# Kernel tuning notes

Hardware: AMD Instinct MI355X
Metric: run time of the kernel (lower is better)

## Reference

```python
import jax, jax.numpy as jnp
import numpy as np

B, N, D, M, C = 4, 256, 128, 128, 128


def _lin_init(key, din, dout):
    # torch nn.Linear default: U(-1/sqrt(din), 1/sqrt(din)) for weight and bias
    bound = 1.0 / np.sqrt(din)
    kw, kb = jax.random.split(key)
    W = jax.random.uniform(kw, (din, dout), jnp.float32, -bound, bound)
    b = jax.random.uniform(kb, (dout,), jnp.float32, -bound, bound)
    return W, b


def setup_inputs() -> dict:
    key = jax.random.key(0)
    k_h, k_adj, k1, k2, k3, k4 = jax.random.split(key, 6)
    h = jax.random.normal(k_h, (B, N, D), jnp.float32)
    adj = jax.random.uniform(k_adj, (B, N, N), jnp.float32)
    # msg MLP: Linear(2D -> M), SiLU, Linear(M -> M). Split first weight into
    # the h_i block (W1a) and h_j block (W1b) of the concatenated input.
    W1, b1 = _lin_init(k1, 2 * D, M)
    W1a, W1b = W1[:D], W1[D:]
    W2, b2 = _lin_init(k2, M, M)
    # to_c MLP: Linear(M -> M), SiLU, Linear(M -> C)
    Wc1, bc1 = _lin_init(k3, M, M)
    Wc2, bc2 = _lin_init(k4, M, C)
    return {"h": h, "adj": adj, "W1a": W1a, "W1b": W1b, "b1": b1,
            "W2": W2, "b2": b2, "Wc1": Wc1, "bc1": bc1, "Wc2": Wc2, "bc2": bc2}


def reference(h, adj, W1a, W1b, b1, W2, b2, Wc1, bc1, Wc2, bc2):
    n = h.shape[1]
    # First msg Linear on cat([h_i, h_j]) == h_i @ W1a + h_j @ W1b + b1.
    # Precompute per-node projections once instead of the (B,N,N,2D) pair tensor.
    pi = jnp.einsum('bnd,dm->bnm', h, W1a)           # (B,N,M) for destination i
    pj = jnp.einsum('bnd,dm->bnm', h, W1b)           # (B,N,M) for source j
    pre = pi[:, :, None, :] + pj[:, None, :, :] + b1  # (B,N,N,M)
    m = jnp.einsum('bijm,mk->bijk', jax.nn.silu(pre), W2) + b2  # (B,N,N,M)
    # zero self-messages (diagonal ignored), then weight by adjacency
    mask = (1.0 - jnp.eye(n, dtype=h.dtype))[None, :, :, None]
    m = m * mask * adj[..., None]
    # mean aggregation over source nodes j with clamped degree
    denom = jnp.clip(jnp.sum(adj, axis=-1, keepdims=True), 1.0)  # (B,N,1)
    m_agg = jnp.sum(m, axis=2) / denom                           # (B,N,M)
    c = jnp.einsum('bnm,mc->bnc', jax.nn.silu(jnp.einsum('bnm,mk->bnk', m_agg, Wc1) + bc1), Wc2) + bc2
    return c
```

## Files before the change

kernel.cpp:

```cpp
#include <hip/hip_runtime.h>
#include <math.h>

#define BB 4
#define NN 256
#define DD 128
#define MM 128
#define CC 128
#define ROWS (BB * NN)
#define RPB 4
#define NBLK (ROWS / RPB)
#define TPB 512

static __device__ __forceinline__ float fast_exp2(float x) {
#if __has_builtin(__builtin_amdgcn_exp2f)
    return __builtin_amdgcn_exp2f(x);
#else
    return __exp2f(x);
#endif
}

static __device__ __forceinline__ float fast_rcp(float x) {
#if __has_builtin(__builtin_amdgcn_rcpf)
    return __builtin_amdgcn_rcpf(x);
#else
    return 1.0f / x;
#endif
}

static __device__ __forceinline__ float silu_f(float x) {
    float e = fast_exp2(-1.44269504088896340736f * x);
    return x * fast_rcp(1.0f + e);
}

__global__ __launch_bounds__(TPB) void k_proj(const float* __restrict__ h,
                                              const float* __restrict__ W1a,
                                              const float* __restrict__ W1b,
                                              const float* __restrict__ b1,
                                              float* __restrict__ pibias,
                                              float* __restrict__ pj) {
    __shared__ float sWa[64 * MM];
    __shared__ float sWb[64 * MM];
    __shared__ float sH[RPB * DD];

    const int t = threadIdx.x;
    const int m = t & 127;
    const int q = t >> 7;
    const int row0 = blockIdx.x * RPB;

    const float bias = b1[m];

    sH[t] = h[(size_t)row0 * DD + t];

    float accA = 0.0f, accB = 0.0f;
    for (int c = 0; c < 2; ++c) {
        __syncthreads();
        const float4* ga = (const float4*)(W1a + (size_t)c * 64 * MM);
        const float4* gb = (const float4*)(W1b + (size_t)c * 64 * MM);
        float4* la = (float4*)sWa;
        float4* lb = (float4*)sWb;
        #pragma unroll
        for (int i = 0; i < 4; ++i) {
            la[t + TPB * i] = ga[t + TPB * i];
            lb[t + TPB * i] = gb[t + TPB * i];
        }
        __syncthreads();

        #pragma unroll 8
        for (int dd = 0; dd < 64; ++dd) {
            const float hv = sH[q * DD + c * 64 + dd];
            accA = fmaf(hv, sWa[dd * MM + m], accA);
            accB = fmaf(hv, sWb[dd * MM + m], accB);
        }
    }

    pibias[(size_t)row0 * MM + t] = accA + bias;
    pj[(size_t)row0 * MM + t]     = accB;
}

__global__ __launch_bounds__(TPB) void k_msgout(const float* __restrict__ adj,
                                                const float* __restrict__ pibias,
                                                const float* __restrict__ pj,
                                                const float* __restrict__ W2,
                                                const float* __restrict__ b2,
                                                const float* __restrict__ Wc1,
                                                const float* __restrict__ bc1,
                                                const float* __restrict__ Wc2,
                                                const float* __restrict__ bc2,
                                                float* __restrict__ out) {
    __shared__ float sStage[64 * MM];
    __shared__ float sAdj[RPB][NN];
    __shared__ float sS[RPB * MM];
    __shared__ float sB[RPB * MM];
    __shared__ float sWred0[8];
    __shared__ float sWred1[8];

    const int t = threadIdx.x;
    const int blk = blockIdx.x;
    const int b = blk >> 6;
    const int i0 = (blk & 63) * RPB;
    const int row0 = b * NN + i0;

    const int m = t & 127;
    const int q = t >> 7;
    const int w = t >> 6;

    const float b2k  = b2[m];
    const float bc1k = bc1[m];
    const float bc2k = bc2[m];
    const float pim  = pibias[(size_t)(row0 + q) * MM + m];

    const float* arow = adj + (size_t)row0 * NN;
    const float a0v = arow[t];
    const float a1v = arow[t + TPB];
    float* sA = &sAdj[0][0];
    sA[t] = a0v;
    sA[t + TPB] = a1v;

    float v0 = a0v, v1 = a1v;
    #pragma unroll
    for (int off = 32; off > 0; off >>= 1) {
        v0 += __shfl_xor(v0, off, 64);
        v1 += __shfl_xor(v1, off, 64);
    }
    if ((t & 63) == 0) { sWred0[w] = v0; sWred1[w] = v1; }
    __syncthreads();

    float A;
    if (q < 2) {
        const int base = (q & 1) * 4;
        A = sWred0[base] + sWred0[base + 1] + sWred0[base + 2] + sWred0[base + 3];
    } else {
        const int base = (q & 1) * 4;
        A = sWred1[base] + sWred1[base + 1] + sWred1[base + 2] + sWred1[base + 3];
    }
    const float aii = sAdj[q][i0 + q];
    __syncthreads();
    if (t < RPB) sAdj[t][i0 + t] = 0.0f;

    const float inv  = 1.0f / fmaxf(A, 1.0f);
    const float bet  = (A - aii) * inv;
    const float npim = -1.44269504088896340736f * pim;

    const float* __restrict__ pjB = pj + (size_t)b * NN * MM;
    float acc = 0.0f;
    for (int c = 0; c < 4; ++c) {
        __syncthreads();
        const float4* g = (const float4*)(pjB + (size_t)c * 64 * MM);
        float4* l = (float4*)sStage;
        #pragma unroll
        for (int i = 0; i < 4; ++i) l[t + TPB * i] = g[t + TPB * i];
        __syncthreads();

        #pragma unroll 8
        for (int jj = 0; jj < 64; ++jj) {
            const float pjv = sStage[jj * MM + m];
            const float wgt = sAdj[q][c * 64 + jj];
            const float x   = pim + pjv;
            const float e   = fast_exp2(fmaf(-1.44269504088896340736f, pjv, npim));
            acc = fmaf(wgt, x * fast_rcp(1.0f + e), acc);
        }
    }
    sS[q * MM + m] = acc * inv;


    float acc2 = bet * b2k;
    for (int c = 0; c < 2; ++c) {
        __syncthreads();
        const float4* g = (const float4*)(W2 + (size_t)c * 64 * MM);
        float4* l = (float4*)sStage;
        #pragma unroll
        for (int i = 0; i < 4; ++i) l[t + TPB * i] = g[t + TPB * i];
        __syncthreads();
        #pragma unroll 8
        for (int dd = 0; dd < 64; ++dd) {
            acc2 = fmaf(sS[q * MM + c * 64 + dd], sStage[dd * MM + m], acc2);
        }
    }
    sB[q * MM + m] = acc2;

    acc2 = bc1k;
    for (int c = 0; c < 2; ++c) {
        __syncthreads();
        const float4* g = (const float4*)(Wc1 + (size_t)c * 64 * MM);
        float4* l = (float4*)sStage;
        #pragma unroll
        for (int i = 0; i < 4; ++i) l[t + TPB * i] = g[t + TPB * i];
        __syncthreads();
        #pragma unroll 8
        for (int dd = 0; dd < 64; ++dd) {
            acc2 = fmaf(sB[q * MM + c * 64 + dd], sStage[dd * MM + m], acc2);
        }
    }
    sS[q * MM + m] = silu_f(acc2);

    acc2 = bc2k;
    for (int c = 0; c < 2; ++c) {
        __syncthreads();
        const float4* g = (const float4*)(Wc2 + (size_t)c * 64 * MM);
        float4* l = (float4*)sStage;
        #pragma unroll
        for (int i = 0; i < 4; ++i) l[t + TPB * i] = g[t + TPB * i];
        __syncthreads();
        #pragma unroll 8
        for (int dd = 0; dd < 64; ++dd) {
            acc2 = fmaf(sS[q * MM + c * 64 + dd], sStage[dd * MM + m], acc2);
        }
    }
    out[(size_t)row0 * CC + t] = acc2;
}

extern "C" void kernel_launch(void* const* d_in, const int* in_sizes, int n_in,
                              void* d_out, int out_size, void* d_ws, size_t ws_size,
                              hipStream_t stream) {
    const float* h   = (const float*)d_in[0];
    const float* adj = (const float*)d_in[1];
    const float* W1a = (const float*)d_in[2];
    const float* W1b = (const float*)d_in[3];
    const float* b1  = (const float*)d_in[4];
    const float* W2  = (const float*)d_in[5];
    const float* b2  = (const float*)d_in[6];
    const float* Wc1 = (const float*)d_in[7];
    const float* bc1 = (const float*)d_in[8];
    const float* Wc2 = (const float*)d_in[9];
    const float* bc2 = (const float*)d_in[10];
    float* out = (float*)d_out;

    float* ws = (float*)d_ws;
    float* pibias = ws;
    float* pj     = ws + (size_t)ROWS * MM;

    k_proj<<<NBLK, TPB, 0, stream>>>(h, W1a, W1b, b1, pibias, pj);
    k_msgout<<<NBLK, TPB, 0, stream>>>(adj, pibias, pj, W2, b2, Wc1, bc1,
                                       Wc2, bc2, out);
}
```

Before: 99.29 us.

## Stage full pj and weights via async global-to-LDS loads, overlapping with compute

Both kernels now stage their whole operand into a large LDS buffer using global_load_lds direct-to-LDS loads, instead of looping over 64-row chunks with a sync pair per chunk. In k_msgout, the next weight matrix (W2, Wc1, Wc2) is prefetched into the half of the buffer no longer being read, so the load overlaps the remaining message or GEMV work. Other changes: self-messages are removed by subtracting the diagonal term instead of zeroing adjacency, and two SiLU reciprocals share a single rcp. The cost is about 130KB of LDS per block, which limits occupancy to one block per CU. Correctness also depends on the async LDS loads having completed before each barrier.

```diff
diff --git a/kernel.cpp b/kernel.cpp
--- a/kernel.cpp
+++ b/kernel.cpp
@@ -11,6 +11,8 @@
 #define NBLK (ROWS / RPB)
 #define TPB 512
 
+#define L2E 1.44269504088896340736f
+
 static __device__ __forceinline__ float fast_exp2(float x) {
 #if __has_builtin(__builtin_amdgcn_exp2f)
     return __builtin_amdgcn_exp2f(x);
@@ -28,8 +30,35 @@
 }
 
 static __device__ __forceinline__ float silu_f(float x) {
-    float e = fast_exp2(-1.44269504088896340736f * x);
+    float e = fast_exp2(-L2E * x);
     return x * fast_rcp(1.0f + e);
+}
+
+#if __has_builtin(__builtin_amdgcn_global_load_lds)
+#define HAS_GLDS 1
+#define GLDS(gp, lp)                                                        \
+    __builtin_amdgcn_global_load_lds(                                       \
+        (const __attribute__((address_space(1))) void*)(gp),                \
+        (__attribute__((address_space(3))) void*)(lp), 16, 0, 0)
+#else
+#define HAS_GLDS 0
+#endif
+
+template <int ITERS>
+static __device__ __forceinline__ void stage_lin(float* lds, const float* g,
+                                                 int t) {
+#if HAS_GLDS
+    const int wv = t >> 6, lane = t & 63;
+    #pragma unroll
+    for (int i = 0; i < ITERS; ++i) {
+        const int c = i * 8 + wv;
+        GLDS(g + (size_t)c * 256 + lane * 4, lds + c * 256);
+    }
+#else
+    #pragma unroll
+    for (int i = 0; i < ITERS; ++i)
+        ((float4*)lds)[i * TPB + t] = ((const float4*)g)[i * TPB + t];
+#endif
 }
 
 __global__ __launch_bounds__(TPB) void k_proj(const float* __restrict__ h,
@@ -38,8 +67,7 @@
                                               const float* __restrict__ b1,
                                               float* __restrict__ pibias,
                                               float* __restrict__ pj) {
-    __shared__ float sWa[64 * MM];
-    __shared__ float sWb[64 * MM];
+    __shared__ float sW[128 * 256];
     __shared__ float sH[RPB * DD];
 
     const int t = threadIdx.x;
@@ -47,30 +75,45 @@
     const int q = t >> 7;
     const int row0 = blockIdx.x * RPB;
 
+    sH[t] = h[(size_t)row0 * DD + t];
+
+#if HAS_GLDS
+    {
+        const int wv = t >> 6, lane = t & 63;
+        #pragma unroll
+        for (int i = 0; i < 16; ++i) {
+            const int r = i * 8 + wv;
+            const float* g = (lane < 32)
+                                 ? (W1a + (size_t)r * 128 + lane * 4)
+                                 : (W1b + (size_t)r * 128 + (lane - 32) * 4);
+            GLDS(g, &sW[r * 256]);
+        }
+    }
+#else
+    #pragma unroll
+    for (int i = 0; i < 16; ++i) {
+        const int f = i * TPB + t;
+        const int r = f >> 6;
+        const int c4 = f & 63;
+        const float4 v = (c4 < 32)
+                             ? ((const float4*)(W1a + (size_t)r * 128))[c4]
+                             : ((const float4*)(W1b + (size_t)r * 128))[c4 - 32];
+        ((float4*)sW)[f] = v;
+    }
+#endif
+
     const float bias = b1[m];
-
-    sH[t] = h[(size_t)row0 * DD + t];
+    __syncthreads();
 
     float accA = 0.0f, accB = 0.0f;
-    for (int c = 0; c < 2; ++c) {
-        __syncthreads();
-        const float4* ga = (const float4*)(W1a + (size_t)c * 64 * MM);
-        const float4* gb = (const float4*)(W1b + (size_t)c * 64 * MM);
-        float4* la = (float4*)sWa;
-        float4* lb = (float4*)sWb;
-        #pragma unroll
-        for (int i = 0; i < 4; ++i) {
-            la[t + TPB * i] = ga[t + TPB * i];
-            lb[t + TPB * i] = gb[t + TPB * i];
-        }
-        __syncthreads();
-
-        #pragma unroll 8
-        for (int dd = 0; dd < 64; ++dd) {
-            const float hv = sH[q * DD + c * 64 + dd];
-            accA = fmaf(hv, sWa[dd * MM + m], accA);
-            accB = fmaf(hv, sWb[dd * MM + m], accB);
-        }
+    const float* sHq = &sH[q * DD];
+    #pragma unroll 8
+    for (int d = 0; d < 128; d += 2) {
+        const float2 hv = *(const float2*)&sHq[d];
+        accA = fmaf(hv.x, sW[d * 256 + m], accA);
+        accB = fmaf(hv.x, sW[d * 256 + 128 + m], accB);
+        accA = fmaf(hv.y, sW[(d + 1) * 256 + m], accA);
+        accB = fmaf(hv.y, sW[(d + 1) * 256 + 128 + m], accB);
     }
 
     pibias[(size_t)row0 * MM + t] = accA + bias;
@@ -87,12 +130,12 @@
                                                 const float* __restrict__ Wc2,
                                                 const float* __restrict__ bc2,
                                                 float* __restrict__ out) {
-    __shared__ float sStage[64 * MM];
+    __shared__ float sPJ[256 * MM];
     __shared__ float sAdj[RPB][NN];
     __shared__ float sS[RPB * MM];
     __shared__ float sB[RPB * MM];
-    __shared__ float sWred0[8];
-    __shared__ float sWred1[8];
+    __shared__ float sWr0[8];
+    __shared__ float sWr1[8];
 
     const int t = threadIdx.x;
     const int blk = blockIdx.x;
@@ -104,10 +147,13 @@
     const int q = t >> 7;
     const int w = t >> 6;
 
+    const float* __restrict__ pjB = pj + (size_t)b * NN * MM;
+    stage_lin<16>(sPJ, pjB, t);
+
+    const float pim  = pibias[(size_t)(row0 + q) * MM + m];
     const float b2k  = b2[m];
     const float bc1k = bc1[m];
     const float bc2k = bc2[m];
-    const float pim  = pibias[(size_t)(row0 + q) * MM + m];
 
     const float* arow = adj + (size_t)row0 * NN;
     const float a0v = arow[t];
@@ -122,88 +168,96 @@
         v0 += __shfl_xor(v0, off, 64);
         v1 += __shfl_xor(v1, off, 64);
     }
-    if ((t & 63) == 0) { sWred0[w] = v0; sWred1[w] = v1; }
+    if ((t & 63) == 0) { sWr0[w] = v0; sWr1[w] = v1; }
+
     __syncthreads();
 
     float A;
-    if (q < 2) {
+    {
         const int base = (q & 1) * 4;
-        A = sWred0[base] + sWred0[base + 1] + sWred0[base + 2] + sWred0[base + 3];
-    } else {
-        const int base = (q & 1) * 4;
-        A = sWred1[base] + sWred1[base + 1] + sWred1[base + 2] + sWred1[base + 3];
+        A = (q < 2) ? (sWr0[base] + sWr0[base + 1] + sWr0[base + 2] + sWr0[base + 3])
+                    : (sWr1[base] + sWr1[base + 1] + sWr1[base + 2] + sWr1[base + 3]);
     }
     const float aii = sAdj[q][i0 + q];
-    __syncthreads();
-    if (t < RPB) sAdj[t][i0 + t] = 0.0f;
-
-    const float inv  = 1.0f / fmaxf(A, 1.0f);
-    const float bet  = (A - aii) * inv;
-    const float npim = -1.44269504088896340736f * pim;
-
-    const float* __restrict__ pjB = pj + (size_t)b * NN * MM;
-    float acc = 0.0f;
-    for (int c = 0; c < 4; ++c) {
-        __syncthreads();
-        const float4* g = (const float4*)(pjB + (size_t)c * 64 * MM);
-        float4* l = (float4*)sStage;
-        #pragma unroll
-        for (int i = 0; i < 4; ++i) l[t + TPB * i] = g[t + TPB * i];
-        __syncthreads();
-
+    const float inv = 1.0f / fmaxf(A, 1.0f);
+    const float bet = (A - aii) * inv;
+    const float npim = -L2E * pim;
+
+    float acc = -aii * silu_f(pim + sPJ[(i0 + q) * MM + m]);
+
+    #pragma unroll 8
+    for (int j = 0; j < 128; j += 2) {
+        const float p0 = sPJ[j * MM + m];
+        const float p1 = sPJ[(j + 1) * MM + m];
+        const float2 wv = *(const float2*)&sAdj[q][j];
+        const float x0 = pim + p0, x1 = pim + p1;
+        const float e0 = fast_exp2(fmaf(-L2E, p0, npim));
+        const float e1 = fast_exp2(fmaf(-L2E, p1, npim));
+        const float d0 = 1.0f + e0, d1 = 1.0f + e1;
+        const float rp = fast_rcp(d0 * d1);
+        acc = fmaf(wv.x * x0, rp * d1, acc);
+        acc = fmaf(wv.y * x1, rp * d0, acc);
+    }
+
+    __syncthreads();
+    stage_lin<8>(sPJ, W2, t);
+
+    #pragma unroll 8
+    for (int j = 128; j < 256; j += 2) {
+        const float p0 = sPJ[j * MM + m];
+        const float p1 = sPJ[(j + 1) * MM + m];
+        const float2 wv = *(const float2*)&sAdj[q][j];
+        const float x0 = pim + p0, x1 = pim + p1;
+        const float e0 = fast_exp2(fmaf(-L2E, p0, npim));
+        const float e1 = fast_exp2(fmaf(-L2E, p1, npim));
+        const float d0 = 1.0f + e0, d1 = 1.0f + e1;
+        const float rp = fast_rcp(d0 * d1);
+        acc = fmaf(wv.x * x0, rp * d1, acc);
+        acc = fmaf(wv.y * x1, rp * d0, acc);
+    }
+    sS[q * MM + m] = acc * inv;
+
+    __syncthreads();
+    stage_lin<8>(sPJ + 16384, Wc1, t);
+
+    float acc2 = bet * b2k;
+    {
+        const float* sSr = &sS[q * MM];
         #pragma unroll 8
-        for (int jj = 0; jj < 64; ++jj) {
-            const float pjv = sStage[jj * MM + m];
-            const float wgt = sAdj[q][c * 64 + jj];
-            const float x   = pim + pjv;
-            const float e   = fast_exp2(fmaf(-1.44269504088896340736f, pjv, npim));
-            acc = fmaf(wgt, x * fast_rcp(1.0f + e), acc);
-        }
-    }
-    sS[q * MM + m] = acc * inv;
-
-
-    float acc2 = bet * b2k;
-    for (int c = 0; c < 2; ++c) {
-        __syncthreads();
-        const float4* g = (const float4*)(W2 + (size_t)c * 64 * MM);
-        float4* l = (float4*)sStage;
-        #pragma unroll
-        for (int i = 0; i < 4; ++i) l[t + TPB * i] = g[t + TPB * i];
-        __syncthreads();
+        for (int d = 0; d < 128; d += 2) {
+            const float2 sv = *(const float2*)&sSr[d];
+            acc2 = fmaf(sv.x, sPJ[d * MM + m], acc2);
+            acc2 = fmaf(sv.y, sPJ[(d + 1) * MM + m], acc2);
+        }
+    }
+    sB[q * MM + m] = acc2;
+
+    __syncthreads();
+    stage_lin<8>(sPJ, Wc2, t);
+
+    acc2 = bc1k;
+    {
+        const float* sBr = &sB[q * MM];
+        const float* sW1 = sPJ + 16384;
         #pragma unroll 8
-        for (int dd = 0; dd < 64; ++dd) {
-            acc2 = fmaf(sS[q * MM + c * 64 + dd], sStage[dd * MM + m], acc2);
-        }
-    }
-    sB[q * MM + m] = acc2;
-
-    acc2 = bc1k;
-    for (int c = 0; c < 2; ++c) {
-        __syncthreads();
-        const float4* g = (const float4*)(Wc1 + (size_t)c * 64 * MM);
-        float4* l = (float4*)sStage;
-        #pragma unroll
-        for (int i = 0; i < 4; ++i) l[t + TPB * i] = g[t + TPB * i];
-        __syncthreads();
+        for (int d = 0; d < 128; d += 2) {
+            const float2 sv = *(const float2*)&sBr[d];
+            acc2 = fmaf(sv.x, sW1[d * MM + m], acc2);
+            acc2 = fmaf(sv.y, sW1[(d + 1) * MM + m], acc2);
+        }
+    }
+    sS[q * MM + m] = silu_f(acc2);
+
+    __syncthreads();
+
+    acc2 = bc2k;
+    {
+        const float* sSr = &sS[q * MM];
         #pragma unroll 8
-        for (int dd = 0; dd < 64; ++dd) {
-            acc2 = fmaf(sB[q * MM + c * 64 + dd], sStage[dd * MM + m], acc2);
-        }
-    }
-    sS[q * MM + m] = silu_f(acc2);
-
-    acc2 = bc2k;
-    for (int c = 0; c < 2; ++c) {
-        __syncthreads();
-        const float4* g = (const float4*)(Wc2 + (size_t)c * 64 * MM);
-        float4* l = (float4*)sStage;
-        #pragma unroll
-        for (int i = 0; i < 4; ++i) l[t + TPB * i] = g[t + TPB * i];
-        __syncthreads();
-        #pragma unroll 8
-        for (int dd = 0; dd < 64; ++dd) {
-            acc2 = fmaf(sS[q * MM + c * 64 + dd], sStage[dd * MM + m], acc2);
+        for (int d = 0; d < 128; d += 2) {
+            const float2 sv = *(const float2*)&sSr[d];
+            acc2 = fmaf(sv.x, sPJ[d * MM + m], acc2);
+            acc2 = fmaf(sv.y, sPJ[(d + 1) * MM + m], acc2);
         }
     }
     out[(size_t)row0 * CC + t] = acc2;
```

New measurement: 97.81 us. About the same (-1.5%).
